# Performance work log

Measured on AMD Instinct MI355X. Metric: run time of the kernel, lower is better.

The kernel has to match this reference:

```python
import jax, jax.numpy as jnp
import numpy as np

NUM_HEADS = 16
D_MODEL = 1024
NEG_INF = -1e30


def setup_inputs() -> dict:
    key = jax.random.key(0)
    ks = jax.random.split(key, 7)
    B, S, D = 2, 2048, D_MODEL
    scale = 1.0 / np.sqrt(D)
    return {
        "queries": jax.random.normal(ks[0], (B, S, D), dtype=jnp.float32),
        "keys": jax.random.normal(ks[1], (B, S, D), dtype=jnp.float32),
        "values": jax.random.normal(ks[2], (B, S, D), dtype=jnp.float32),
        "Wq": jax.random.normal(ks[3], (D, D), dtype=jnp.float32) * scale,
        "Wk": jax.random.normal(ks[4], (D, D), dtype=jnp.float32) * scale,
        "Wv": jax.random.normal(ks[5], (D, D), dtype=jnp.float32) * scale,
        "Wo": jax.random.normal(ks[6], (D, D), dtype=jnp.float32) * scale,
    }


def _split_heads(x, h):
    # [B, S, D] -> [B, h, S, D/h]
    B, S, D = x.shape
    return x.reshape(B, S, h, D // h).transpose(0, 2, 1, 3)


def reference(queries, keys, values, Wq, Wk, Wv, Wo):
    h = NUM_HEADS
    q = _split_heads(queries @ Wq, h)  # [B, h, S, dh]
    k = _split_heads(keys @ Wk, h)
    v = _split_heads(values @ Wv, h)
    dh = q.shape[-1]
    scores = jnp.einsum("bhqd,bhkd->bhqk", q, k) / jnp.sqrt(jnp.float32(dh))
    # original quirk: exactly-zero scores are masked to -1e30 before softmax
    scores = jnp.where(scores == 0, NEG_INF, scores)
    attn = jax.nn.softmax(scores, axis=-1)
    out = jnp.einsum("bhqk,bhkd->bhqd", attn, v)  # [B, h, S, dh]
    B, _, S, _ = out.shape
    out = out.transpose(0, 2, 1, 3).reshape(B, S, h * dh)
    return out @ Wo
```

## Files before the change

### kernel.cpp

```cpp
#include <hip/hip_runtime.h>

typedef unsigned short u16;
typedef short bf16x8 __attribute__((ext_vector_type(8)));
typedef float f32x4 __attribute__((ext_vector_type(4)));
typedef float f32x16 __attribute__((ext_vector_type(16)));

namespace {

constexpr int kB = 2, kS = 2048, kD = 1024, kH = 16, kDh = 64;
constexpr float kC2 = 0.125f * 1.44269504088896341f;

__device__ inline u16 f32_bf16(float f) {
    unsigned u = __float_as_uint(f);
    u += 0x7FFFu + ((u >> 16) & 1u);
    return (u16)(u >> 16);
}

__device__ inline u16 f32_bf16_fast(float f) {
    return (u16)((__float_as_uint(f) + 0x8000u) >> 16);
}

__device__ inline float fast_exp2(float x) {
    float r;
    asm("v_exp_f32 %0, %1" : "=v"(r) : "v"(x));
    return r;
}

__device__ inline void gl_lds16(const void* g, void* l) {
    __builtin_amdgcn_global_load_lds(
        (const __attribute__((address_space(1))) void*)g,
        (__attribute__((address_space(3))) void*)l, 16, 0, 0);
}

__device__ inline int swz8(int l) {
    return ((l & 3) ^ ((l >> 2) & 3) ^ ((l >> 4) & 3)) * 8;
}

__global__ __launch_bounds__(256) void prep(
    const float* __restrict__ s0, const float* __restrict__ s1,
    const float* __restrict__ s2,
    u16* __restrict__ d0, u16* __restrict__ d1, u16* __restrict__ d2,
    const float* __restrict__ W0, const float* __restrict__ W1,
    const float* __restrict__ W2, const float* __restrict__ W3,
    u16* __restrict__ T0, u16* __restrict__ T1,
    u16* __restrict__ T2, u16* __restrict__ T3)
{
    const int y = blockIdx.y;
    if (y < 3) {
        const float* src = y == 0 ? s0 : (y == 1 ? s1 : s2);
        u16* dst = y == 0 ? d0 : (y == 1 ? d1 : d2);
        const int i = blockIdx.x * 256 + threadIdx.x;
        const float4* s4 = (const float4*)src;
        float4 a = s4[2 * i], b = s4[2 * i + 1];
        uint4 o;
        o.x = (unsigned)f32_bf16(a.x) | ((unsigned)f32_bf16(a.y) << 16);
        o.y = (unsigned)f32_bf16(a.z) | ((unsigned)f32_bf16(a.w) << 16);
        o.z = (unsigned)f32_bf16(b.x) | ((unsigned)f32_bf16(b.y) << 16);
        o.w = (unsigned)f32_bf16(b.z) | ((unsigned)f32_bf16(b.w) << 16);
        ((uint4*)dst)[i] = o;
        return;
    }
    if (blockIdx.x >= 256) return;
    const int z = y - 3;
    const float* W = z == 0 ? W0 : (z == 1 ? W1 : (z == 2 ? W2 : W3));
    u16* Wt = z == 0 ? T0 : (z == 1 ? T1 : (z == 2 ? T2 : T3));
    const float sc = (z == 0) ? kC2 : 1.0f;

    __shared__ __attribute__((aligned(16))) u16 T[64][65];
    const int t = threadIdx.x;
    const int n0 = (blockIdx.x & 15) * 64, k0 = (blockIdx.x >> 4) * 64;
    const int r = t >> 4, c4 = (t & 15) * 4;
#pragma unroll
    for (int it = 0; it < 4; ++it) {
        const int rr = r + 16 * it;
        float4 v = *(const float4*)(W + (size_t)(k0 + rr) * kD + n0 + c4);
        T[rr][c4 + 0] = f32_bf16(v.x * sc);
        T[rr][c4 + 1] = f32_bf16(v.y * sc);
        T[rr][c4 + 2] = f32_bf16(v.z * sc);
        T[rr][c4 + 3] = f32_bf16(v.w * sc);
    }
    __syncthreads();
#pragma unroll
    for (int it = 0; it < 4; ++it) {
        const int nn = r + 16 * it;
        uint2 pk;
        pk.x = (unsigned)T[c4 + 0][nn] | ((unsigned)T[c4 + 1][nn] << 16);
        pk.y = (unsigned)T[c4 + 2][nn] | ((unsigned)T[c4 + 3][nn] << 16);
        *(uint2*)(Wt + (size_t)(n0 + nn) * kD + k0 + c4) = pk;
    }
}

__global__ __launch_bounds__(256) void vtrans(
    const u16* __restrict__ V, u16* __restrict__ Vt)
{
    __shared__ __attribute__((aligned(16))) u16 T[64][65];
    const int t = threadIdx.x;
    const int s0 = blockIdx.x * 64;
    const int bh = blockIdx.y, b = bh >> 4, h = bh & 15;
    const int rr = t >> 3, c0 = (t & 7) * 8;
    union { u16 u[8]; uint4 v4; } buf;
#pragma unroll
    for (int p = 0; p < 2; ++p) {
        const int s = rr + 32 * p;
        buf.v4 = *(const uint4*)(V + (size_t)(b * kS + s0 + s) * kD + h * kDh + c0);
#pragma unroll
        for (int i = 0; i < 8; ++i) T[c0 + i][s] = buf.u[i];
    }
    __syncthreads();
#pragma unroll
    for (int p = 0; p < 2; ++p) {
        const int d = rr + 32 * p;
#pragma unroll
        for (int i = 0; i < 8; ++i) buf.u[i] = T[d][c0 + i];
        *(uint4*)(Vt + (size_t)(bh * kDh + d) * kS + s0 + c0) = buf.v4;
    }
}

template <bool F32OUT>
__device__ inline void gemm128_body(
    const u16* __restrict__ A, const u16* __restrict__ Wt,
    void* __restrict__ Cout, int M, int N, int K, int bx, int by)
{
    __shared__ __attribute__((aligned(16))) u16 As[128 * 32];
    __shared__ __attribute__((aligned(16))) u16 Bs[128 * 32];
    const int t = threadIdx.x, w = t >> 6, l = t & 63;
    const int quad = l >> 4, c = l & 15;
    const int wm = w >> 1, wn = w & 1;
    const int m0 = by * 128, n0 = bx * 128;
    const int lr = l >> 2, lc = swz8(l);
    const int xc = ((quad ^ (c & 3) ^ ((c >> 2) & 3))) * 8;

    const u16* ga0 = A  + (size_t)(m0 + w * 32 + lr) * K + lc;
    const u16* ga1 = A  + (size_t)(m0 + w * 32 + 16 + lr) * K + lc;
    const u16* gb0 = Wt + (size_t)(n0 + w * 32 + lr) * K + lc;
    const u16* gb1 = Wt + (size_t)(n0 + w * 32 + 16 + lr) * K + lc;
    u16* la0 = &As[(w * 32) * 32];
    u16* la1 = &As[(w * 32 + 16) * 32];
    u16* lb0 = &Bs[(w * 32) * 32];
    u16* lb1 = &Bs[(w * 32 + 16) * 32];

    f32x4 acc[4][4];
#pragma unroll
    for (int mi = 0; mi < 4; ++mi)
#pragma unroll
        for (int nj = 0; nj < 4; ++nj) acc[mi][nj] = 0;

    for (int k0 = 0; k0 < K; k0 += 32) {
        gl_lds16(ga0 + k0, la0);
        gl_lds16(ga1 + k0, la1);
        gl_lds16(gb0 + k0, lb0);
        gl_lds16(gb1 + k0, lb1);
        __syncthreads();
        bf16x8 af[4], bf[4];
#pragma unroll
        for (int mi = 0; mi < 4; ++mi)
            af[mi] = *(const bf16x8*)&As[(wm * 64 + mi * 16 + c) * 32 + xc];
#pragma unroll
        for (int nj = 0; nj < 4; ++nj)
            bf[nj] = *(const bf16x8*)&Bs[(wn * 64 + nj * 16 + c) * 32 + xc];
#pragma unroll
        for (int mi = 0; mi < 4; ++mi)
#pragma unroll
            for (int nj = 0; nj < 4; ++nj)
                acc[mi][nj] = __builtin_amdgcn_mfma_f32_16x16x32_bf16(
                    af[mi], bf[nj], acc[mi][nj], 0, 0, 0);
        __syncthreads();
    }

#pragma unroll
    for (int mi = 0; mi < 4; ++mi)
#pragma unroll
        for (int nj = 0; nj < 4; ++nj)
#pragma unroll
            for (int r = 0; r < 4; ++r) {
                const size_t row = m0 + wm * 64 + mi * 16 + quad * 4 + r;
                const size_t col = n0 + wn * 64 + nj * 16 + c;
                if (F32OUT)
                    ((float*)Cout)[row * N + col] = acc[mi][nj][r];
                else
                    ((u16*)Cout)[row * N + col] = f32_bf16(acc[mi][nj][r]);
            }
}

__global__ __launch_bounds__(256) void gemm_qkv(
    const u16* __restrict__ A0, const u16* __restrict__ A1,
    const u16* __restrict__ A2,
    const u16* __restrict__ W0, const u16* __restrict__ W1,
    const u16* __restrict__ W2,
    u16* __restrict__ C0, u16* __restrict__ C1, u16* __restrict__ C2)
{
    const int z = blockIdx.z;
    const u16* A  = z == 0 ? A0 : (z == 1 ? A1 : A2);
    const u16* Wt = z == 0 ? W0 : (z == 1 ? W1 : W2);
    u16* C = z == 0 ? C0 : (z == 1 ? C1 : C2);
    gemm128_body<false>(A, Wt, C, kB * kS, kD, kD, blockIdx.x, blockIdx.y);
}

__global__ __launch_bounds__(256) void gemm_out(
    const u16* __restrict__ A, const u16* __restrict__ Wt,
    float* __restrict__ C)
{
    __shared__ __attribute__((aligned(16))) u16 As[64 * 32];
    __shared__ __attribute__((aligned(16))) u16 Bs[128 * 32];
    const int N = kD, K = kD;
    const int t = threadIdx.x, w = t >> 6, l = t & 63;
    const int quad = l >> 4, c = l & 15;
    const int wm = w >> 1, wn = w & 1;
    const int m0 = blockIdx.y * 64, n0 = blockIdx.x * 128;
    const int lr = l >> 2, lc = swz8(l);
    const int xc = ((quad ^ (c & 3) ^ ((c >> 2) & 3))) * 8;

    const u16* ga  = A  + (size_t)(m0 + w * 16 + lr) * K + lc;
    const u16* gb0 = Wt + (size_t)(n0 + w * 16 + lr) * K + lc;
    const u16* gb1 = Wt + (size_t)(n0 + 64 + w * 16 + lr) * K + lc;
    u16* la  = &As[(w * 16) * 32];
    u16* lb0 = &Bs[(w * 16) * 32];
    u16* lb1 = &Bs[(64 + w * 16) * 32];

    f32x4 acc[2][4];
#pragma unroll
    for (int mi = 0; mi < 2; ++mi)
#pragma unroll
        for (int nj = 0; nj < 4; ++nj) acc[mi][nj] = 0;

    for (int k0 = 0; k0 < K; k0 += 32) {
        gl_lds16(ga + k0, la);
        gl_lds16(gb0 + k0, lb0);
        gl_lds16(gb1 + k0, lb1);
        __syncthreads();
        bf16x8 af[2], bf[4];
#pragma unroll
        for (int mi = 0; mi < 2; ++mi)
            af[mi] = *(const bf16x8*)&As[(wm * 32 + mi * 16 + c) * 32 + xc];
#pragma unroll
        for (int nj = 0; nj < 4; ++nj)
            bf[nj] = *(const bf16x8*)&Bs[(wn * 64 + nj * 16 + c) * 32 + xc];
#pragma unroll
        for (int mi = 0; mi < 2; ++mi)
#pragma unroll
            for (int nj = 0; nj < 4; ++nj)
                acc[mi][nj] = __builtin_amdgcn_mfma_f32_16x16x32_bf16(
                    af[mi], bf[nj], acc[mi][nj], 0, 0, 0);
        __syncthreads();
    }

#pragma unroll
    for (int mi = 0; mi < 2; ++mi)
#pragma unroll
        for (int nj = 0; nj < 4; ++nj)
#pragma unroll
            for (int r = 0; r < 4; ++r) {
                const size_t row = m0 + wm * 32 + mi * 16 + quad * 4 + r;
                const size_t col = n0 + wn * 64 + nj * 16 + c;
                C[row * N + col] = acc[mi][nj][r];
            }
}

__global__ __launch_bounds__(256) void attn(
    const u16* __restrict__ Q, const u16* __restrict__ K,
    const u16* __restrict__ Vt, u16* __restrict__ AO)
{
    __shared__ __attribute__((aligned(16))) u16 KsL[64 * 64];
    __shared__ __attribute__((aligned(16))) u16 VtL[64 * 64];
    __shared__ __attribute__((aligned(16))) u16 QPs[4 * 32 * 64];

    const int t = threadIdx.x, w = t >> 6, l = t & 63;
    const int half = l >> 5, m = l & 31;
    const int q0 = blockIdx.x * 128;
    const int bh = blockIdx.y, b = bh >> 4, h = bh & 15;
    const int sl = l >> 3;
    const int sc = (l & 7) ^ sl;
    const int cc = l & 7;
    const int R0w = w * 16;

    const size_t kbase = (size_t)(b * kS) * kD + h * kDh;
    const size_t vbase = (size_t)bh * kDh * kS;
    const size_t qbase = (size_t)(b * kS + q0 + w * 32) * kD + h * kDh;

#pragma unroll
    for (int i = 0; i < 4; ++i)
        gl_lds16(Q + qbase + (size_t)(i * 8 + sl) * kD + sc * 8,
                 &QPs[w * 2048 + i * 512]);

    uint4 kreg[2], vreg[2];
#pragma unroll
    for (int i = 0; i < 2; ++i) {
        kreg[i] = *(const uint4*)(K + kbase + (size_t)(R0w + i * 8 + sl) * kD + sc * 8);
        vreg[i] = *(const uint4*)(Vt + vbase + (size_t)(R0w + i * 8 + sl) * kS + sc * 8);
    }
#pragma unroll
    for (int i = 0; i < 2; ++i) {
        *(uint4*)&KsL[(R0w + i * 8 + sl) * 64 + cc * 8] = kreg[i];
        *(uint4*)&VtL[(R0w + i * 8 + sl) * 64 + cc * 8] = vreg[i];
    }
    __syncthreads();

    bf16x8 qf[4];
#pragma unroll
    for (int ch = 0; ch < 4; ++ch)
        qf[ch] = *(const bf16x8*)
            &QPs[w * 2048 + m * 64 + ((2 * ch + half) ^ (m & 7)) * 8];

    bf16x8 ones;
#pragma unroll
    for (int i = 0; i < 8; ++i) ones[i] = (short)0x3F80;

    f32x16 o0 = 0, o1 = 0, ol = 0;
    constexpr int NT = kS / 64;

    for (int kt = 0; kt < NT; ++kt) {
        if (kt + 1 < NT) {
#pragma unroll
            for (int i = 0; i < 2; ++i) {
                kreg[i] = *(const uint4*)
                    (K + kbase + (size_t)((kt + 1) * 64 + R0w + i * 8 + sl) * kD + sc * 8);
                vreg[i] = *(const uint4*)
                    (Vt + vbase + (size_t)(R0w + i * 8 + sl) * kS + (kt + 1) * 64 + sc * 8);
            }
        }

        f32x16 s0 = 0, s1 = 0;
#pragma unroll
        for (int ch = 0; ch < 4; ++ch) {
            const int xo = ((2 * ch + half) ^ (m & 7)) * 8;
            const bf16x8 kf0 = *(const bf16x8*)&KsL[(m) * 64 + xo];
            const bf16x8 kf1 = *(const bf16x8*)&KsL[(32 + m) * 64 + xo];
            s0 = __builtin_amdgcn_mfma_f32_32x32x16_bf16(qf[ch], kf0, s0, 0, 0, 0);
            s1 = __builtin_amdgcn_mfma_f32_32x32x16_bf16(qf[ch], kf1, s1, 0, 0, 0);
        }

#pragma unroll
        for (int reg = 0; reg < 16; ++reg) {
            const int qrow = (reg & 3) + 8 * (reg >> 2) + 4 * half;
            const int base = w * 2048 + qrow * 64;
            const int sw = (qrow & 7);
            {
                const int key = m;
                QPs[base + ((key >> 3) ^ sw) * 8 + (key & 7)] =
                    f32_bf16_fast(fast_exp2(s0[reg]));
            }
            {
                const int key = 32 + m;
                QPs[base + ((key >> 3) ^ sw) * 8 + (key & 7)] =
                    f32_bf16_fast(fast_exp2(s1[reg]));
            }
        }

#pragma unroll
        for (int ch = 0; ch < 4; ++ch) {
            const int xo = ((2 * ch + half) ^ (m & 7)) * 8;
            const bf16x8 pf = *(const bf16x8*)&QPs[w * 2048 + m * 64 + xo];
            const bf16x8 vf0 = *(const bf16x8*)&VtL[(m) * 64 + xo];
            const bf16x8 vf1 = *(const bf16x8*)&VtL[(32 + m) * 64 + xo];
            o0 = __builtin_amdgcn_mfma_f32_32x32x16_bf16(pf, vf0, o0, 0, 0, 0);
            o1 = __builtin_amdgcn_mfma_f32_32x32x16_bf16(pf, vf1, o1, 0, 0, 0);
            ol = __builtin_amdgcn_mfma_f32_32x32x16_bf16(pf, ones, ol, 0, 0, 0);
        }

        if (kt + 1 < NT) {
            __syncthreads();
#pragma unroll
            for (int i = 0; i < 2; ++i) {
                *(uint4*)&KsL[(R0w + i * 8 + sl) * 64 + cc * 8] = kreg[i];
                *(uint4*)&VtL[(R0w + i * 8 + sl) * 64 + cc * 8] = vreg[i];
            }
            __syncthreads();
        }
    }

    const size_t obase = (size_t)(b * kS + q0 + w * 32) * kD + h * kDh;
#pragma unroll
    for (int reg = 0; reg < 16; ++reg) {
        const int qrow = (reg & 3) + 8 * (reg >> 2) + 4 * half;
        const float inv = 1.0f / ol[reg];
        AO[obase + (size_t)qrow * kD + m]      = f32_bf16(o0[reg] * inv);
        AO[obase + (size_t)qrow * kD + 32 + m] = f32_bf16(o1[reg] * inv);
    }
}

}

extern "C" void kernel_launch(void* const* d_in, const int* in_sizes, int n_in,
                              void* d_out, int out_size, void* d_ws, size_t ws_size,
                              hipStream_t stream)
{
    const float* q_in = (const float*)d_in[0];
    const float* k_in = (const float*)d_in[1];
    const float* v_in = (const float*)d_in[2];
    const float* Wq   = (const float*)d_in[3];
    const float* Wk   = (const float*)d_in[4];
    const float* Wv   = (const float*)d_in[5];
    const float* Wo   = (const float*)d_in[6];

    u16* ws = (u16*)d_ws;
    const size_t M1 = 1u << 20;
    u16* xq  = ws;
    u16* xk  = ws + 4 * M1;
    u16* xv  = ws + 8 * M1;
    u16* Wtq = ws + 12 * M1;
    u16* Wtk = ws + 13 * M1;
    u16* Wtv = ws + 14 * M1;
    u16* Wto = ws + 15 * M1;
    u16* Qp  = ws + 16 * M1;
    u16* Kp  = ws + 20 * M1;
    u16* Vp  = ws + 24 * M1;
    u16* AO  = ws + 28 * M1;
    u16* Vtg = xq;

    hipLaunchKernelGGL(prep, dim3(2048, 7), dim3(256), 0, stream,
                       q_in, k_in, v_in, xq, xk, xv,
                       Wq, Wk, Wv, Wo, Wtq, Wtk, Wtv, Wto);

    hipLaunchKernelGGL(gemm_qkv, dim3(8, 32, 3), dim3(256), 0, stream,
                       xq, xk, xv, Wtq, Wtk, Wtv, Qp, Kp, Vp);

    hipLaunchKernelGGL(vtrans, dim3(32, 32), dim3(256), 0, stream, Vp, Vtg);

    hipLaunchKernelGGL(attn, dim3(16, 32), dim3(256), 0, stream, Qp, Kp, Vtg, AO);

    hipLaunchKernelGGL(gemm_out, dim3(8, 64), dim3(256), 0, stream,
                       AO, Wto, (float*)d_out);
}
```

Baseline: 252.6 us.

## Make attention single-wave per block with direct-to-LDS K/V loads, no barriers

The attention kernel moves from 256-thread blocks, where four waves share K/V tiles and synchronise through barriers, to 64-thread single-wave blocks covering 32 query rows each. Each wave now loads its own K and V tiles straight into LDS with global-to-LDS loads and waits on vmcnt, removing all __syncthreads and the register-staged prefetch. This launches four times as many blocks and aims to hide latency through more resident blocks per CU instead of intra-block double buffering. In exchange, K/V loads are no longer shared across waves, so L2/global traffic per query row rises, and each tile load is exposed within the wave because nothing prefetches the next tile.

```diff
diff --git a/kernel.cpp b/kernel.cpp
--- a/kernel.cpp
+++ b/kernel.cpp
@@ -256,50 +256,34 @@
             }
 }
 
-__global__ __launch_bounds__(256) void attn(
+__global__ __launch_bounds__(64) void attn(
     const u16* __restrict__ Q, const u16* __restrict__ K,
     const u16* __restrict__ Vt, u16* __restrict__ AO)
 {
     __shared__ __attribute__((aligned(16))) u16 KsL[64 * 64];
     __shared__ __attribute__((aligned(16))) u16 VtL[64 * 64];
-    __shared__ __attribute__((aligned(16))) u16 QPs[4 * 32 * 64];
-
-    const int t = threadIdx.x, w = t >> 6, l = t & 63;
+    __shared__ __attribute__((aligned(16))) u16 QPs[32 * 64];
+
+    const int l = threadIdx.x;
     const int half = l >> 5, m = l & 31;
-    const int q0 = blockIdx.x * 128;
+    const int q0 = blockIdx.x * 32;
     const int bh = blockIdx.y, b = bh >> 4, h = bh & 15;
     const int sl = l >> 3;
     const int sc = (l & 7) ^ sl;
-    const int cc = l & 7;
-    const int R0w = w * 16;
 
     const size_t kbase = (size_t)(b * kS) * kD + h * kDh;
     const size_t vbase = (size_t)bh * kDh * kS;
-    const size_t qbase = (size_t)(b * kS + q0 + w * 32) * kD + h * kDh;
+    const size_t qbase = (size_t)(b * kS + q0) * kD + h * kDh;
 
 #pragma unroll
     for (int i = 0; i < 4; ++i)
-        gl_lds16(Q + qbase + (size_t)(i * 8 + sl) * kD + sc * 8,
-                 &QPs[w * 2048 + i * 512]);
-
-    uint4 kreg[2], vreg[2];
-#pragma unroll
-    for (int i = 0; i < 2; ++i) {
-        kreg[i] = *(const uint4*)(K + kbase + (size_t)(R0w + i * 8 + sl) * kD + sc * 8);
-        vreg[i] = *(const uint4*)(Vt + vbase + (size_t)(R0w + i * 8 + sl) * kS + sc * 8);
-    }
-#pragma unroll
-    for (int i = 0; i < 2; ++i) {
-        *(uint4*)&KsL[(R0w + i * 8 + sl) * 64 + cc * 8] = kreg[i];
-        *(uint4*)&VtL[(R0w + i * 8 + sl) * 64 + cc * 8] = vreg[i];
-    }
-    __syncthreads();
+        gl_lds16(Q + qbase + (size_t)(i * 8 + sl) * kD + sc * 8, &QPs[i * 512]);
+    asm volatile("s_waitcnt vmcnt(0)" ::: "memory");
 
     bf16x8 qf[4];
 #pragma unroll
     for (int ch = 0; ch < 4; ++ch)
-        qf[ch] = *(const bf16x8*)
-            &QPs[w * 2048 + m * 64 + ((2 * ch + half) ^ (m & 7)) * 8];
+        qf[ch] = *(const bf16x8*)&QPs[m * 64 + ((2 * ch + half) ^ (m & 7)) * 8];
 
     bf16x8 ones;
 #pragma unroll
@@ -309,15 +293,14 @@
     constexpr int NT = kS / 64;
 
     for (int kt = 0; kt < NT; ++kt) {
-        if (kt + 1 < NT) {
-#pragma unroll
-            for (int i = 0; i < 2; ++i) {
-                kreg[i] = *(const uint4*)
-                    (K + kbase + (size_t)((kt + 1) * 64 + R0w + i * 8 + sl) * kD + sc * 8);
-                vreg[i] = *(const uint4*)
-                    (Vt + vbase + (size_t)(R0w + i * 8 + sl) * kS + (kt + 1) * 64 + sc * 8);
-            }
+#pragma unroll
+        for (int i = 0; i < 8; ++i) {
+            gl_lds16(K + kbase + (size_t)(kt * 64 + i * 8 + sl) * kD + sc * 8,
+                     &KsL[i * 512]);
+            gl_lds16(Vt + vbase + (size_t)(i * 8 + sl) * kS + kt * 64 + sc * 8,
+                     &VtL[i * 512]);
         }
+        asm volatile("s_waitcnt vmcnt(0)" ::: "memory");
 
         f32x16 s0 = 0, s1 = 0;
 #pragma unroll
@@ -332,7 +315,7 @@
 #pragma unroll
         for (int reg = 0; reg < 16; ++reg) {
             const int qrow = (reg & 3) + 8 * (reg >> 2) + 4 * half;
-            const int base = w * 2048 + qrow * 64;
+            const int base = qrow * 64;
             const int sw = (qrow & 7);
             {
                 const int key = m;
@@ -349,26 +332,16 @@
 #pragma unroll
         for (int ch = 0; ch < 4; ++ch) {
             const int xo = ((2 * ch + half) ^ (m & 7)) * 8;
-            const bf16x8 pf = *(const bf16x8*)&QPs[w * 2048 + m * 64 + xo];
+            const bf16x8 pf = *(const bf16x8*)&QPs[m * 64 + xo];
             const bf16x8 vf0 = *(const bf16x8*)&VtL[(m) * 64 + xo];
             const bf16x8 vf1 = *(const bf16x8*)&VtL[(32 + m) * 64 + xo];
             o0 = __builtin_amdgcn_mfma_f32_32x32x16_bf16(pf, vf0, o0, 0, 0, 0);
             o1 = __builtin_amdgcn_mfma_f32_32x32x16_bf16(pf, vf1, o1, 0, 0, 0);
             ol = __builtin_amdgcn_mfma_f32_32x32x16_bf16(pf, ones, ol, 0, 0, 0);
         }
-
-        if (kt + 1 < NT) {
-            __syncthreads();
-#pragma unroll
-            for (int i = 0; i < 2; ++i) {
-                *(uint4*)&KsL[(R0w + i * 8 + sl) * 64 + cc * 8] = kreg[i];
-                *(uint4*)&VtL[(R0w + i * 8 + sl) * 64 + cc * 8] = vreg[i];
-            }
-            __syncthreads();
-        }
-    }
-
-    const size_t obase = (size_t)(b * kS + q0 + w * 32) * kD + h * kDh;
+    }
+
+    const size_t obase = (size_t)(b * kS + q0) * kD + h * kDh;
 #pragma unroll
     for (int reg = 0; reg < 16; ++reg) {
         const int qrow = (reg & 3) + 8 * (reg >> 2) + 4 * half;
@@ -416,7 +389,7 @@
 
     hipLaunchKernelGGL(vtrans, dim3(32, 32), dim3(256), 0, stream, Vp, Vtg);
 
-    hipLaunchKernelGGL(attn, dim3(16, 32), dim3(256), 0, stream, Qp, Kp, Vtg, AO);
+    hipLaunchKernelGGL(attn, dim3(64, 32), dim3(64), 0, stream, Qp, Kp, Vtg, AO);
 
     hipLaunchKernelGGL(gemm_out, dim3(8, 64), dim3(256), 0, stream,
                        AO, Wto, (float*)d_out);
```

Result: faster. 246.7 us (-2.4%).

## Load K/V tiles directly to LDS with global_load_lds instead of register prefetch

Applied to the files above, without the earlier changes.

Replaces the register-staged software prefetch of the next K and Vt tiles with direct global-to-LDS loads issued at the start of each iteration, followed by a barrier. The Q and P buffers are split into separate shared arrays so the Q staging area is no longer reused for probabilities. This removes register pressure and the extra LDS store instructions, but the load of each tile is no longer overlapped with compute on the previous tile, which risks exposing memory latency.

```diff
diff --git a/kernel.cpp b/kernel.cpp
--- a/kernel.cpp
+++ b/kernel.cpp
@@ -262,7 +262,8 @@
 {
     __shared__ __attribute__((aligned(16))) u16 KsL[64 * 64];
     __shared__ __attribute__((aligned(16))) u16 VtL[64 * 64];
-    __shared__ __attribute__((aligned(16))) u16 QPs[4 * 32 * 64];
+    __shared__ __attribute__((aligned(16))) u16 Qs[4 * 32 * 64];
+    __shared__ __attribute__((aligned(16))) u16 Ps[4 * 32 * 64];
 
     const int t = threadIdx.x, w = t >> 6, l = t & 63;
     const int half = l >> 5, m = l & 31;
@@ -270,54 +271,39 @@
     const int bh = blockIdx.y, b = bh >> 4, h = bh & 15;
     const int sl = l >> 3;
     const int sc = (l & 7) ^ sl;
-    const int cc = l & 7;
-    const int R0w = w * 16;
+
+    const size_t qbase = (size_t)(b * kS + q0 + w * 32) * kD + h * kDh;
+#pragma unroll
+    for (int i = 0; i < 4; ++i)
+        gl_lds16(Q + qbase + (size_t)(i * 8 + sl) * kD + sc * 8,
+                 &Qs[w * 2048 + i * 512]);
+    __syncthreads();
+
+    bf16x8 qf[4];
+#pragma unroll
+    for (int ch = 0; ch < 4; ++ch)
+        qf[ch] = *(const bf16x8*)
+            &Qs[w * 2048 + m * 64 + ((2 * ch + half) ^ (m & 7)) * 8];
+
+    bf16x8 ones;
+#pragma unroll
+    for (int i = 0; i < 8; ++i) ones[i] = (short)0x3F80;
+
+    f32x16 o0 = 0, o1 = 0, ol = 0;
 
     const size_t kbase = (size_t)(b * kS) * kD + h * kDh;
     const size_t vbase = (size_t)bh * kDh * kS;
-    const size_t qbase = (size_t)(b * kS + q0 + w * 32) * kD + h * kDh;
-
-#pragma unroll
-    for (int i = 0; i < 4; ++i)
-        gl_lds16(Q + qbase + (size_t)(i * 8 + sl) * kD + sc * 8,
-                 &QPs[w * 2048 + i * 512]);
-
-    uint4 kreg[2], vreg[2];
-#pragma unroll
-    for (int i = 0; i < 2; ++i) {
-        kreg[i] = *(const uint4*)(K + kbase + (size_t)(R0w + i * 8 + sl) * kD + sc * 8);
-        vreg[i] = *(const uint4*)(Vt + vbase + (size_t)(R0w + i * 8 + sl) * kS + sc * 8);
-    }
-#pragma unroll
-    for (int i = 0; i < 2; ++i) {
-        *(uint4*)&KsL[(R0w + i * 8 + sl) * 64 + cc * 8] = kreg[i];
-        *(uint4*)&VtL[(R0w + i * 8 + sl) * 64 + cc * 8] = vreg[i];
-    }
-    __syncthreads();
-
-    bf16x8 qf[4];
-#pragma unroll
-    for (int ch = 0; ch < 4; ++ch)
-        qf[ch] = *(const bf16x8*)
-            &QPs[w * 2048 + m * 64 + ((2 * ch + half) ^ (m & 7)) * 8];
-
-    bf16x8 ones;
-#pragma unroll
-    for (int i = 0; i < 8; ++i) ones[i] = (short)0x3F80;
-
-    f32x16 o0 = 0, o1 = 0, ol = 0;
-    constexpr int NT = kS / 64;
-
-    for (int kt = 0; kt < NT; ++kt) {
-        if (kt + 1 < NT) {
-#pragma unroll
-            for (int i = 0; i < 2; ++i) {
-                kreg[i] = *(const uint4*)
-                    (K + kbase + (size_t)((kt + 1) * 64 + R0w + i * 8 + sl) * kD + sc * 8);
-                vreg[i] = *(const uint4*)
-                    (Vt + vbase + (size_t)(R0w + i * 8 + sl) * kS + (kt + 1) * 64 + sc * 8);
-            }
+
+    for (int kt = 0; kt < kS / 64; ++kt) {
+#pragma unroll
+        for (int i = 0; i < 2; ++i) {
+            const int R0 = w * 16 + i * 8;
+            gl_lds16(K + kbase + (size_t)(kt * 64 + R0 + sl) * kD + sc * 8,
+                     &KsL[R0 * 64]);
+            gl_lds16(Vt + vbase + (size_t)(R0 + sl) * kS + kt * 64 + sc * 8,
+                     &VtL[R0 * 64]);
         }
+        __syncthreads();
 
         f32x16 s0 = 0, s1 = 0;
 #pragma unroll
@@ -336,12 +322,12 @@
             const int sw = (qrow & 7);
             {
                 const int key = m;
-                QPs[base + ((key >> 3) ^ sw) * 8 + (key & 7)] =
+                Ps[base + ((key >> 3) ^ sw) * 8 + (key & 7)] =
                     f32_bf16_fast(fast_exp2(s0[reg]));
             }
             {
                 const int key = 32 + m;
-                QPs[base + ((key >> 3) ^ sw) * 8 + (key & 7)] =
+                Ps[base + ((key >> 3) ^ sw) * 8 + (key & 7)] =
                     f32_bf16_fast(fast_exp2(s1[reg]));
             }
         }
@@ -349,23 +335,14 @@
 #pragma unroll
         for (int ch = 0; ch < 4; ++ch) {
             const int xo = ((2 * ch + half) ^ (m & 7)) * 8;
-            const bf16x8 pf = *(const bf16x8*)&QPs[w * 2048 + m * 64 + xo];
+            const bf16x8 pf = *(const bf16x8*)&Ps[w * 2048 + m * 64 + xo];
             const bf16x8 vf0 = *(const bf16x8*)&VtL[(m) * 64 + xo];
             const bf16x8 vf1 = *(const bf16x8*)&VtL[(32 + m) * 64 + xo];
             o0 = __builtin_amdgcn_mfma_f32_32x32x16_bf16(pf, vf0, o0, 0, 0, 0);
             o1 = __builtin_amdgcn_mfma_f32_32x32x16_bf16(pf, vf1, o1, 0, 0, 0);
             ol = __builtin_amdgcn_mfma_f32_32x32x16_bf16(pf, ones, ol, 0, 0, 0);
         }
-
-        if (kt + 1 < NT) {
-            __syncthreads();
-#pragma unroll
-            for (int i = 0; i < 2; ++i) {
-                *(uint4*)&KsL[(R0w + i * 8 + sl) * 64 + cc * 8] = kreg[i];
-                *(uint4*)&VtL[(R0w + i * 8 + sl) * 64 + cc * 8] = vreg[i];
-            }
-            __syncthreads();
-        }
+        __syncthreads();
     }
 
     const size_t obase = (size_t)(b * kS + q0 + w * 32) * kD + h * kDh;
```

Measured after the change: 231.9 us. 8.2% less time.
